# Kernel optimization log

Measured on AMD Instinct MI355X. Metric: run time of the kernel, lower is better.

## Reference

```python
import jax, jax.numpy as jnp
from jax import lax
import numpy as np

CONF_THR = 1e-4   # confidence_threshold
NMS_THR = 0.5     # nms_threshold


def haar2d(x):
    # x: [N, H, W] -> LL, LH, HL, HH each [N, H//2, W//2] (single-level Haar DWT)
    a = x[:, 0::2, 0::2]
    b = x[:, 0::2, 1::2]
    c = x[:, 1::2, 0::2]
    d = x[:, 1::2, 1::2]
    LL = (a + b + c + d) * 0.5
    LH = (a + b - c - d) * 0.5
    HL = (a - b + c - d) * 0.5
    HH = (a - b - c + d) * 0.5
    return LL, LH, HL, HH


def nms_keep(boxes, masked_scores, valid, nms_thr):
    # Greedy NMS, faithful to the torch while-loop: process in descending score
    # order; a box is kept iff not suppressed by an earlier kept box with IoU > thr.
    N = boxes.shape[0]
    order = jnp.argsort(-masked_scores)
    b = boxes[order]
    v = valid[order]
    x1, y1, x2, y2 = b[:, 0], b[:, 1], b[:, 2], b[:, 3]
    areas = (x2 - x1) * (y2 - y1)
    idx = jnp.arange(N)

    def body(i, st):
        sup, keep = st
        cur = jnp.logical_and(jnp.logical_not(sup[i]), v[i])
        keep = keep.at[i].set(cur)
        xx1 = jnp.maximum(x1, x1[i])
        yy1 = jnp.maximum(y1, y1[i])
        xx2 = jnp.minimum(x2, x2[i])
        yy2 = jnp.minimum(y2, y2[i])
        inter = jnp.maximum(xx2 - xx1, 0.0) * jnp.maximum(yy2 - yy1, 0.0)
        iou = inter / (areas[i] + areas - inter)
        sup = sup | (cur & (iou > nms_thr) & (idx > i))
        return sup, keep

    sup0 = jnp.logical_not(v)  # invalid boxes never kept
    keep0 = jnp.zeros((N,), dtype=bool)
    _, keep_sorted = lax.fori_loop(0, N, body, (sup0, keep0))
    # map back to original box order
    return jnp.zeros((N,), dtype=bool).at[order].set(keep_sorted)


def reference(boxes, scores, logits, features, labels):
    N = boxes.shape[0]
    # wavelet decomposition of per-detection feature maps
    LL, LH, HL, HH = haar2d(features)

    # detection quality = confidence * max softmax prob * box geometry quality
    max_prob = jnp.max(jax.nn.softmax(logits, axis=-1), axis=-1)
    w = boxes[:, 2] - boxes[:, 0]
    h = boxes[:, 3] - boxes[:, 1]
    aspect = jnp.minimum(w / h, h / w)
    area = w * h
    area_score = jnp.clip(area / (jnp.max(area) + 1e-6), 0.0, 1.0)
    det_quality = scores * max_prob * (aspect * area_score)

    # feature quality: feature bank is empty at init -> ones (exact initial-state semantics)
    feat_quality = jnp.ones((N,), dtype=boxes.dtype)

    # edge quality from high-frequency subbands (mean |.| over flattened subband dim)
    h_edge = jnp.mean(jnp.abs(LH.reshape(N, -1)), axis=1)
    v_edge = jnp.mean(jnp.abs(HL.reshape(N, -1)), axis=1)
    d_edge = jnp.mean(jnp.abs(HH.reshape(N, -1)), axis=1)
    edge_quality = (h_edge + v_edge + d_edge) / 3.0

    quality = det_quality * 0.4 + feat_quality * 0.3 + edge_quality * 0.3

    valid = quality > CONF_THR
    masked_scores = jnp.where(valid, scores, -jnp.inf)
    keep = nms_keep(lax.stop_gradient(boxes), lax.stop_gradient(masked_scores), valid, NMS_THR)

    # fixed-shape output: [N,6] = (boxes, score, quality) zeroed where not kept
    out = jnp.concatenate([boxes, scores[:, None], quality[:, None]], axis=1)
    out = out * keep[:, None].astype(out.dtype)
    return out, keep, labels


def setup_inputs() -> dict:
    key = jax.random.key(0)
    k1, k2, k3, k4, k5, k6 = jax.random.split(key, 6)
    N, C, H, W = 8192, 1000, 64, 64
    cxcy = jax.random.uniform(k1, (N, 2), dtype=jnp.float32) * 1000.0
    wh = jax.random.uniform(k2, (N, 2), dtype=jnp.float32) * 100.0 + 1.0
    boxes = jnp.concatenate([cxcy - wh / 2, cxcy + wh / 2], axis=1)
    scores = jax.random.uniform(k3, (N,), dtype=jnp.float32)
    logits = jax.random.normal(k4, (N, C), dtype=jnp.float32) * 3.0
    features = jax.random.normal(k5, (N, H, W), dtype=jnp.float32)
    labels = jax.random.randint(k6, (N,), 0, C)
    return {"boxes": boxes, "scores": scores, "logits": logits, "features": features, "labels": labels}
```

## Files before the change

### kernel.cpp

```cpp
#include <hip/hip_runtime.h>

#pragma clang fp contract(off)

typedef unsigned long long u64;
typedef unsigned int u32;

#define NB 8192
#define NW 128
#define EMAX 16384

#define OFF_EDGEQ 0
#define OFF_MP    (OFF_EDGEQ + NB * 4)
#define OFF_Q     (OFF_MP    + NB * 4)
#define OFF_KEEP  (OFF_Q     + NB * 4)
#define OFF_ECNT  (OFF_KEEP  + NW * 8)
#define OFF_EDGES (OFF_ECNT  + 256)

__device__ __forceinline__ float haar3(float a, float b, float c, float d) {
    return fabsf(a + b - c - d) + fabsf(a - b + c - d) + fabsf(a - b - c + d);
}

__global__ __launch_bounds__(256) void k_edge(const float* __restrict__ feat,
                                              float* __restrict__ edgeq) {
    int n = blockIdx.x;
    const float* f = feat + (size_t)n * 4096;
    int t = threadIdx.x;
    int hr = t >> 3, g = t & 7;
    const float4* row0 = (const float4*)(f + (2 * hr) * 64);
    const float4* row1 = (const float4*)(f + (2 * hr) * 64 + 64);
    float4 e0 = row0[g];
    float4 e1 = row0[8 + g];
    float4 o0 = row1[g];
    float4 o1 = row1[8 + g];
    float s = haar3(e0.x, e0.y, o0.x, o0.y) + haar3(e0.z, e0.w, o0.z, o0.w)
            + haar3(e1.x, e1.y, o1.x, o1.y) + haar3(e1.z, e1.w, o1.z, o1.w);
    for (int off = 32; off; off >>= 1) s += __shfl_down(s, off, 64);
    __shared__ float wsum[4];
    int wv = t >> 6, ln = t & 63;
    if (ln == 0) wsum[wv] = s;
    __syncthreads();
    if (t == 0) edgeq[n] = (wsum[0] + wsum[1] + wsum[2] + wsum[3]) * (0.5f / 3072.0f);
}

__global__ __launch_bounds__(256) void k_logit(const float* __restrict__ logits,
                                               float* __restrict__ mp) {
    int wave = threadIdx.x >> 6, lane = threadIdx.x & 63;
    int row = blockIdx.x * 4 + wave;
    const float4* p = (const float4*)(logits + (size_t)row * 1000);
    float4 v0 = p[lane];
    float4 v1 = p[lane + 64];
    float4 v2 = p[lane + 128];
    bool has3 = (lane + 192) < 250;
    float4 v3 = p[has3 ? (lane + 192) : lane];
    float m = fmaxf(fmaxf(fmaxf(v0.x, v0.y), fmaxf(v0.z, v0.w)),
                    fmaxf(fmaxf(v1.x, v1.y), fmaxf(v1.z, v1.w)));
    m = fmaxf(m, fmaxf(fmaxf(v2.x, v2.y), fmaxf(v2.z, v2.w)));
    if (has3) m = fmaxf(m, fmaxf(fmaxf(v3.x, v3.y), fmaxf(v3.z, v3.w)));
    for (int off = 32; off; off >>= 1) m = fmaxf(m, __shfl_xor(m, off, 64));
    float s = expf(v0.x - m) + expf(v0.y - m) + expf(v0.z - m) + expf(v0.w - m)
            + expf(v1.x - m) + expf(v1.y - m) + expf(v1.z - m) + expf(v1.w - m)
            + expf(v2.x - m) + expf(v2.y - m) + expf(v2.z - m) + expf(v2.w - m);
    if (has3) s += expf(v3.x - m) + expf(v3.y - m) + expf(v3.z - m) + expf(v3.w - m);
    for (int off = 32; off; off >>= 1) s += __shfl_xor(s, off, 64);
    if (lane == 0) mp[row] = 1.0f / s;
}

__global__ __launch_bounds__(1024) void k_quality(const float* __restrict__ boxes,
        const float* __restrict__ scores, const float* __restrict__ edgeq,
        const float* __restrict__ mp, float* __restrict__ quality,
        u32* __restrict__ ecnt) {
    int tid = threadIdx.x;
    if (tid == 0) *ecnt = 0;
    float amax = 0.f;
    float areaLoc[8];
    #pragma unroll
    for (int t = 0; t < 8; ++t) {
        int i = tid + t * 1024;
        float4 b = ((const float4*)boxes)[i];
        float w = b.z - b.x, h = b.w - b.y;
        areaLoc[t] = w * h;
        amax = fmaxf(amax, areaLoc[t]);
    }
    for (int off = 32; off; off >>= 1) amax = fmaxf(amax, __shfl_xor(amax, off, 64));
    __shared__ float wmax[16];
    int wv = tid >> 6, ln = tid & 63;
    if (ln == 0) wmax[wv] = amax;
    __syncthreads();
    if (tid == 0) {
        float mm = wmax[0];
        for (int k = 1; k < 16; ++k) mm = fmaxf(mm, wmax[k]);
        wmax[0] = mm;
    }
    __syncthreads();
    float maxA = wmax[0];
    #pragma unroll
    for (int t = 0; t < 8; ++t) {
        int i = tid + t * 1024;
        float4 b = ((const float4*)boxes)[i];
        float w = b.z - b.x, h = b.w - b.y;
        float aspect = fminf(w / h, h / w);
        float ascore = areaLoc[t] / (maxA + 1e-6f);
        ascore = fminf(fmaxf(ascore, 0.f), 1.f);
        float det = scores[i] * mp[i] * (aspect * ascore);
        quality[i] = det * 0.4f + 0.3f + edgeq[i] * 0.3f;
    }
}

__global__ __launch_bounds__(64) void k_mat(const float* __restrict__ boxes,
        const float* __restrict__ scores, u32* __restrict__ ecnt,
        u32* __restrict__ edges) {
    int jt = blockIdx.x, it = blockIdx.y;
    if (jt < it) return;
    int lane = threadIdx.x;
    __shared__ float cx1[64], cy1[64], cx2[64], cy2[64], car[64], csc[64];
    int j0 = jt * 64;
    {
        float4 bj = ((const float4*)boxes)[j0 + lane];
        cx1[lane] = bj.x; cy1[lane] = bj.y; cx2[lane] = bj.z; cy2[lane] = bj.w;
        car[lane] = (bj.z - bj.x) * (bj.w - bj.y);
        csc[lane] = scores[j0 + lane];
    }
    __syncthreads();
    int i = it * 64 + lane;
    float4 bi = ((const float4*)boxes)[i];
    float X1 = bi.x, Y1 = bi.y, X2 = bi.z, Y2 = bi.w;
    float AR = (bi.z - bi.x) * (bi.w - bi.y);
    float SI = scores[i];
    bool diag = (jt == it);
    #pragma unroll 4
    for (int b = 0; b < 64; ++b) {
        if (diag && b <= lane) continue;
        float xx1 = fmaxf(cx1[b], X1);
        float yy1 = fmaxf(cy1[b], Y1);
        float xx2 = fminf(cx2[b], X2);
        float yy2 = fminf(cy2[b], Y2);
        float iw = fmaxf(xx2 - xx1, 0.0f);
        float ih = fmaxf(yy2 - yy1, 0.0f);
        float inter = iw * ih;
        float denom = (AR + car[b]) - inter;
        if (inter > 0.25f * denom) {
            float iou = inter / denom;
            if (iou > 0.5f) {
                int j = j0 + b;
                float SJ = csc[b];
                bool ihi = (SI > SJ) || (SI == SJ && i < j);
                u32 hi = ihi ? (u32)i : (u32)j;
                u32 lo = ihi ? (u32)j : (u32)i;
                u32 pos = atomicAdd(ecnt, 1u);
                if (pos < EMAX) edges[pos] = (hi << 16) | lo;
            }
        }
    }
}

__global__ __launch_bounds__(256) void k_scan4(const u32* __restrict__ ecnt,
        const u32* __restrict__ edges, u64* __restrict__ keepm) {
    __shared__ u64 dec[NW], kept[NW], keptIn[NW], pendIn[NW];
    __shared__ int undec;
    int tid = threadIdx.x;
    if (tid < NW) { dec[tid] = 0; kept[tid] = 0; }
    int E = (int)min(*ecnt, (u32)EMAX);
    __syncthreads();
    for (int round = 0; round < NB; ++round) {
        if (tid < NW) { keptIn[tid] = 0; pendIn[tid] = 0; }
        if (tid == 0) undec = 0;
        __syncthreads();
        for (int e = tid; e < E; e += 256) {
            u32 pk = edges[e];
            int hi = (int)(pk >> 16), lo = (int)(pk & 0xFFFFu);
            bool d = (dec[hi >> 6] >> (hi & 63)) & 1ull;
            bool k = (kept[hi >> 6] >> (hi & 63)) & 1ull;
            if (!d)     atomicOr(&pendIn[lo >> 6], 1ull << (lo & 63));
            else if (k) atomicOr(&keptIn[lo >> 6], 1ull << (lo & 63));
        }
        __syncthreads();
        if (tid < NW) {
            u64 und = ~dec[tid];
            u64 sup = und & keptIn[tid];
            u64 kp  = und & ~keptIn[tid] & ~pendIn[tid];
            kept[tid] |= kp;
            dec[tid]  |= sup | kp;
            if (und & ~(sup | kp)) undec = 1;
        }
        __syncthreads();
        if (!undec) break;
    }
    if (tid < NW) keepm[tid] = kept[tid];
}

__global__ __launch_bounds__(256) void k_out(const float* __restrict__ boxes,
        const float* __restrict__ scores, const float* __restrict__ quality,
        const u64* __restrict__ keepmask, const int* __restrict__ labels,
        float* __restrict__ out) {
    int n = blockIdx.x * 256 + threadIdx.x;
    bool kept = (keepmask[n >> 6] >> (n & 63)) & 1ull;
    float kf = kept ? 1.0f : 0.0f;
    float4 b = ((const float4*)boxes)[n];
    float* o = out + (size_t)n * 6;
    o[0] = b.x * kf; o[1] = b.y * kf; o[2] = b.z * kf; o[3] = b.w * kf;
    o[4] = scores[n] * kf;
    o[5] = quality[n] * kf;
    out[6 * NB + n] = kf;
    out[7 * NB + n] = (float)labels[n];
}

extern "C" void kernel_launch(void* const* d_in, const int* in_sizes, int n_in,
                              void* d_out, int out_size, void* d_ws, size_t ws_size,
                              hipStream_t stream) {
    const float* boxes  = (const float*)d_in[0];
    const float* scores = (const float*)d_in[1];
    const float* logits = (const float*)d_in[2];
    const float* feats  = (const float*)d_in[3];
    const int*   labels = (const int*)d_in[4];
    float* out = (float*)d_out;
    char* ws = (char*)d_ws;

    float* edgeq  = (float*)(ws + OFF_EDGEQ);
    float* mp     = (float*)(ws + OFF_MP);
    float* qual   = (float*)(ws + OFF_Q);
    u64*   keepm  = (u64*)(ws + OFF_KEEP);
    u32*   ecnt   = (u32*)(ws + OFF_ECNT);
    u32*   edges  = (u32*)(ws + OFF_EDGES);

    k_edge<<<NB, 256, 0, stream>>>(feats, edgeq);
    k_logit<<<NB / 4, 256, 0, stream>>>(logits, mp);
    k_quality<<<1, 1024, 0, stream>>>(boxes, scores, edgeq, mp, qual, ecnt);
    dim3 gmat(NW, NW);
    k_mat<<<gmat, 64, 0, stream>>>(boxes, scores, ecnt, edges);
    k_scan4<<<1, 256, 0, stream>>>(ecnt, edges, keepm);
    k_out<<<NB / 256, 256, 0, stream>>>(boxes, scores, qual, keepm, labels, out);
}
```

Measured before the change: 121.8 us.

## Use nontemporal loads, fast exp, 4-wave IoU blocks and LDS-cached edge list

Streaming loads of the features and logits now use nontemporal hints, and the softmax uses __expf in place of expf. The quality kernel caches aspect ratios instead of reloading boxes. The IoU matrix kernel packs four 64-column tiles per 256-thread block, cutting the block count and early-exit overhead. The NMS scan copies up to 12288 edges into LDS so the repeated rounds read shared memory instead of global memory. The cost is slightly different exp rounding and a large LDS footprint in the single-block scan.

Result: no change. 121.3 us (-0.5%).

```diff
diff --git a/kernel.cpp b/kernel.cpp
--- a/kernel.cpp
+++ b/kernel.cpp
@@ -4,10 +4,12 @@
 
 typedef unsigned long long u64;
 typedef unsigned int u32;
+typedef float f32x4 __attribute__((ext_vector_type(4)));
 
 #define NB 8192
 #define NW 128
 #define EMAX 16384
+#define ELDS 12288
 
 #define OFF_EDGEQ 0
 #define OFF_MP    (OFF_EDGEQ + NB * 4)
@@ -15,6 +17,11 @@
 #define OFF_KEEP  (OFF_Q     + NB * 4)
 #define OFF_ECNT  (OFF_KEEP  + NW * 8)
 #define OFF_EDGES (OFF_ECNT  + 256)
+
+__device__ __forceinline__ float4 ldnt4(const float4* p) {
+    f32x4 v = __builtin_nontemporal_load((const f32x4*)p);
+    return make_float4(v.x, v.y, v.z, v.w);
+}
 
 __device__ __forceinline__ float haar3(float a, float b, float c, float d) {
     return fabsf(a + b - c - d) + fabsf(a - b + c - d) + fabsf(a - b - c + d);
@@ -28,10 +35,10 @@
     int hr = t >> 3, g = t & 7;
     const float4* row0 = (const float4*)(f + (2 * hr) * 64);
     const float4* row1 = (const float4*)(f + (2 * hr) * 64 + 64);
-    float4 e0 = row0[g];
-    float4 e1 = row0[8 + g];
-    float4 o0 = row1[g];
-    float4 o1 = row1[8 + g];
+    float4 e0 = ldnt4(row0 + g);
+    float4 e1 = ldnt4(row0 + 8 + g);
+    float4 o0 = ldnt4(row1 + g);
+    float4 o1 = ldnt4(row1 + 8 + g);
     float s = haar3(e0.x, e0.y, o0.x, o0.y) + haar3(e0.z, e0.w, o0.z, o0.w)
             + haar3(e1.x, e1.y, o1.x, o1.y) + haar3(e1.z, e1.w, o1.z, o1.w);
     for (int off = 32; off; off >>= 1) s += __shfl_down(s, off, 64);
@@ -47,20 +54,20 @@
     int wave = threadIdx.x >> 6, lane = threadIdx.x & 63;
     int row = blockIdx.x * 4 + wave;
     const float4* p = (const float4*)(logits + (size_t)row * 1000);
-    float4 v0 = p[lane];
-    float4 v1 = p[lane + 64];
-    float4 v2 = p[lane + 128];
+    float4 v0 = ldnt4(p + lane);
+    float4 v1 = ldnt4(p + lane + 64);
+    float4 v2 = ldnt4(p + lane + 128);
     bool has3 = (lane + 192) < 250;
-    float4 v3 = p[has3 ? (lane + 192) : lane];
+    float4 v3 = ldnt4(p + (has3 ? (lane + 192) : lane));
     float m = fmaxf(fmaxf(fmaxf(v0.x, v0.y), fmaxf(v0.z, v0.w)),
                     fmaxf(fmaxf(v1.x, v1.y), fmaxf(v1.z, v1.w)));
     m = fmaxf(m, fmaxf(fmaxf(v2.x, v2.y), fmaxf(v2.z, v2.w)));
     if (has3) m = fmaxf(m, fmaxf(fmaxf(v3.x, v3.y), fmaxf(v3.z, v3.w)));
     for (int off = 32; off; off >>= 1) m = fmaxf(m, __shfl_xor(m, off, 64));
-    float s = expf(v0.x - m) + expf(v0.y - m) + expf(v0.z - m) + expf(v0.w - m)
-            + expf(v1.x - m) + expf(v1.y - m) + expf(v1.z - m) + expf(v1.w - m)
-            + expf(v2.x - m) + expf(v2.y - m) + expf(v2.z - m) + expf(v2.w - m);
-    if (has3) s += expf(v3.x - m) + expf(v3.y - m) + expf(v3.z - m) + expf(v3.w - m);
+    float s = __expf(v0.x - m) + __expf(v0.y - m) + __expf(v0.z - m) + __expf(v0.w - m)
+            + __expf(v1.x - m) + __expf(v1.y - m) + __expf(v1.z - m) + __expf(v1.w - m)
+            + __expf(v2.x - m) + __expf(v2.y - m) + __expf(v2.z - m) + __expf(v2.w - m);
+    if (has3) s += __expf(v3.x - m) + __expf(v3.y - m) + __expf(v3.z - m) + __expf(v3.w - m);
     for (int off = 32; off; off >>= 1) s += __shfl_xor(s, off, 64);
     if (lane == 0) mp[row] = 1.0f / s;
 }
@@ -72,13 +79,14 @@
     int tid = threadIdx.x;
     if (tid == 0) *ecnt = 0;
     float amax = 0.f;
-    float areaLoc[8];
+    float areaLoc[8], aspLoc[8];
     #pragma unroll
     for (int t = 0; t < 8; ++t) {
         int i = tid + t * 1024;
         float4 b = ((const float4*)boxes)[i];
         float w = b.z - b.x, h = b.w - b.y;
         areaLoc[t] = w * h;
+        aspLoc[t] = fminf(w / h, h / w);
         amax = fmaxf(amax, areaLoc[t]);
     }
     for (int off = 32; off; off >>= 1) amax = fmaxf(amax, __shfl_xor(amax, off, 64));
@@ -96,31 +104,33 @@
     #pragma unroll
     for (int t = 0; t < 8; ++t) {
         int i = tid + t * 1024;
-        float4 b = ((const float4*)boxes)[i];
-        float w = b.z - b.x, h = b.w - b.y;
-        float aspect = fminf(w / h, h / w);
         float ascore = areaLoc[t] / (maxA + 1e-6f);
         ascore = fminf(fmaxf(ascore, 0.f), 1.f);
-        float det = scores[i] * mp[i] * (aspect * ascore);
+        float det = scores[i] * mp[i] * (aspLoc[t] * ascore);
         quality[i] = det * 0.4f + 0.3f + edgeq[i] * 0.3f;
     }
 }
 
-__global__ __launch_bounds__(64) void k_mat(const float* __restrict__ boxes,
+__global__ __launch_bounds__(256) void k_mat(const float* __restrict__ boxes,
         const float* __restrict__ scores, u32* __restrict__ ecnt,
         u32* __restrict__ edges) {
-    int jt = blockIdx.x, it = blockIdx.y;
-    if (jt < it) return;
-    int lane = threadIdx.x;
-    __shared__ float cx1[64], cy1[64], cx2[64], cy2[64], car[64], csc[64];
+    int it = blockIdx.y;
+    if ((int)blockIdx.x * 4 + 3 < it) return;
+    int wv = threadIdx.x >> 6, lane = threadIdx.x & 63;
+    int jt = blockIdx.x * 4 + wv;
+    bool active = (jt >= it);
+    __shared__ float sh[4][6][64];
+    if (active) {
+        int j0 = jt * 64;
+        float4 bj = ((const float4*)boxes)[j0 + lane];
+        sh[wv][0][lane] = bj.x; sh[wv][1][lane] = bj.y;
+        sh[wv][2][lane] = bj.z; sh[wv][3][lane] = bj.w;
+        sh[wv][4][lane] = (bj.z - bj.x) * (bj.w - bj.y);
+        sh[wv][5][lane] = scores[j0 + lane];
+    }
+    __syncthreads();
+    if (!active) return;
     int j0 = jt * 64;
-    {
-        float4 bj = ((const float4*)boxes)[j0 + lane];
-        cx1[lane] = bj.x; cy1[lane] = bj.y; cx2[lane] = bj.z; cy2[lane] = bj.w;
-        car[lane] = (bj.z - bj.x) * (bj.w - bj.y);
-        csc[lane] = scores[j0 + lane];
-    }
-    __syncthreads();
     int i = it * 64 + lane;
     float4 bi = ((const float4*)boxes)[i];
     float X1 = bi.x, Y1 = bi.y, X2 = bi.z, Y2 = bi.w;
@@ -130,19 +140,19 @@
     #pragma unroll 4
     for (int b = 0; b < 64; ++b) {
         if (diag && b <= lane) continue;
-        float xx1 = fmaxf(cx1[b], X1);
-        float yy1 = fmaxf(cy1[b], Y1);
-        float xx2 = fminf(cx2[b], X2);
-        float yy2 = fminf(cy2[b], Y2);
+        float xx1 = fmaxf(sh[wv][0][b], X1);
+        float yy1 = fmaxf(sh[wv][1][b], Y1);
+        float xx2 = fminf(sh[wv][2][b], X2);
+        float yy2 = fminf(sh[wv][3][b], Y2);
         float iw = fmaxf(xx2 - xx1, 0.0f);
         float ih = fmaxf(yy2 - yy1, 0.0f);
         float inter = iw * ih;
-        float denom = (AR + car[b]) - inter;
+        float denom = (AR + sh[wv][4][b]) - inter;
         if (inter > 0.25f * denom) {
             float iou = inter / denom;
             if (iou > 0.5f) {
                 int j = j0 + b;
-                float SJ = csc[b];
+                float SJ = sh[wv][5][b];
                 bool ihi = (SI > SJ) || (SI == SJ && i < j);
                 u32 hi = ihi ? (u32)i : (u32)j;
                 u32 lo = ihi ? (u32)j : (u32)i;
@@ -156,17 +166,19 @@
 __global__ __launch_bounds__(256) void k_scan4(const u32* __restrict__ ecnt,
         const u32* __restrict__ edges, u64* __restrict__ keepm) {
     __shared__ u64 dec[NW], kept[NW], keptIn[NW], pendIn[NW];
+    __shared__ u32 eL[ELDS];
     __shared__ int undec;
     int tid = threadIdx.x;
+    int E = (int)min(*ecnt, (u32)EMAX);
     if (tid < NW) { dec[tid] = 0; kept[tid] = 0; }
-    int E = (int)min(*ecnt, (u32)EMAX);
+    for (int e = tid; e < E && e < ELDS; e += 256) eL[e] = edges[e];
     __syncthreads();
     for (int round = 0; round < NB; ++round) {
         if (tid < NW) { keptIn[tid] = 0; pendIn[tid] = 0; }
         if (tid == 0) undec = 0;
         __syncthreads();
         for (int e = tid; e < E; e += 256) {
-            u32 pk = edges[e];
+            u32 pk = (e < ELDS) ? eL[e] : edges[e];
             int hi = (int)(pk >> 16), lo = (int)(pk & 0xFFFFu);
             bool d = (dec[hi >> 6] >> (hi & 63)) & 1ull;
             bool k = (kept[hi >> 6] >> (hi & 63)) & 1ull;
@@ -225,8 +237,8 @@
     k_edge<<<NB, 256, 0, stream>>>(feats, edgeq);
     k_logit<<<NB / 4, 256, 0, stream>>>(logits, mp);
     k_quality<<<1, 1024, 0, stream>>>(boxes, scores, edgeq, mp, qual, ecnt);
-    dim3 gmat(NW, NW);
-    k_mat<<<gmat, 64, 0, stream>>>(boxes, scores, ecnt, edges);
+    dim3 gmat(32, NW);
+    k_mat<<<gmat, 256, 0, stream>>>(boxes, scores, ecnt, edges);
     k_scan4<<<1, 256, 0, stream>>>(ecnt, edges, keepm);
     k_out<<<NB / 256, 256, 0, stream>>>(boxes, scores, qual, keepm, labels, out);
 }
```
